# Optimization experiments

Measured on AMD Instinct MI355X. Metric: run time of the kernel, lower is better.

## Reference

```python
import jax, jax.numpy as jnp
import numpy as np

BATCH = 131072
FEAS = 256
K = 256
DEPTH = 3


def setup_inputs() -> dict:
    key = jax.random.key(0)
    ks = jax.random.split(key, 16)
    # deep tower dims: k//1 -> k//2 -> k//3 -> k//4  == 256 -> 128 -> 85 -> 64
    dims = [K // i for i in range(1, DEPTH + 2)]
    inp = {
        "x": jax.random.normal(ks[0], (BATCH, FEAS), jnp.float32),
        "w_wide": jax.random.normal(ks[1], (FEAS, 1), jnp.float32) * 0.02,
        "b_wide": jnp.zeros((1,), jnp.float32),
        # nn.Parameter(torch.rand(feas, k)) -> uniform [0,1)
        "V": jax.random.uniform(ks[2], (FEAS, K), jnp.float32),
    }
    for i in range(DEPTH):
        fan_in, fan_out = dims[i], dims[i + 1]
        inp[f"w{i+1}"] = jax.random.normal(ks[3 + 2 * i], (fan_in, fan_out), jnp.float32) * (1.0 / np.sqrt(fan_in))
        inp[f"b{i+1}"] = jnp.zeros((fan_out,), jnp.float32)
    inp["w_out"] = jax.random.normal(ks[12], (dims[-1], 1), jnp.float32) * (1.0 / np.sqrt(dims[-1]))
    inp["b_out"] = jnp.zeros((1,), jnp.float32)
    return inp


def reference(x, w_wide, b_wide, V, w1, b1, w2, b2, w3, b3, w_out, b_out):
    # wide (linear) part: [B, 1]
    linear = x @ w_wide + b_wide
    # FM bi-interaction pooling. Original loop: sum_{j >= i} x_i x_j (v_i * v_j)
    # (break/continue on zeros only skip zero-valued terms). Including the
    # diagonal, this equals 0.5 * ((x @ V)^2 + (x^2) @ (V^2)).  [B, K]
    xv = x @ V
    x2v2 = (x * x) @ (V * V)
    tmp = 0.5 * (xv * xv + x2v2)
    # deep tower: Linear + ReLU at each depth
    for w, b in ((w1, b1), (w2, b2), (w3, b3)):
        tmp = jax.nn.relu(tmp @ w + b)
    deep_out = tmp @ w_out + b_out  # [B, 1]
    return jax.nn.sigmoid(linear + deep_out)
```

## Files before the change

kernel.cpp:

```cpp
#include <hip/hip_runtime.h>
#include <math.h>


typedef _Float16 f16;
typedef _Float16 f16x4 __attribute__((ext_vector_type(4)));
typedef _Float16 f16x8 __attribute__((ext_vector_type(8)));
typedef float f32x4 __attribute__((ext_vector_type(4)));

#define NROWS   131072
#define ROWS    64
#define FDIM    256
#define KDIM    256
#define D1      128
#define D2      85
#define D2P     96

#define OFF_VT_H   0x0UL
#define OFF_VT_L   0x20000UL
#define OFF_V2T    0x40000UL
#define OFF_W1T_H  0x60000UL
#define OFF_W1T_L  0x70000UL
#define OFF_W2T_H  0x80000UL
#define OFF_W2T_L  0x86000UL
#define OFF_W3T_H  0x8C000UL
#define OFF_W3T_L  0x8F000UL

static __device__ __forceinline__ f32x4 mfma16(f16x8 a, f16x8 b, f32x4 c) {
  return __builtin_amdgcn_mfma_f32_16x16x32_f16(a, b, c, 0, 0, 0);
}

__global__ __launch_bounds__(256) void prep_kernel(
    const float* __restrict__ V, const float* __restrict__ w1,
    const float* __restrict__ w2, const float* __restrict__ w3,
    f16* VT_h, f16* VT_l, f16* V2T,
    f16* W1T_h, f16* W1T_l, f16* W2T_h, f16* W2T_l, f16* W3T_h, f16* W3T_l) {
  int idx0 = blockIdx.x * 256 + threadIdx.x;
  int stride = gridDim.x * 256;
  for (int idx = idx0; idx < KDIM * FDIM; idx += stride) {
    int k = idx >> 8, i = idx & 255;
    float v = V[i * KDIM + k];
    f16 h = (f16)v;
    VT_h[idx] = h;
    VT_l[idx] = (f16)(v - (float)h);
    V2T[idx] = (f16)(v * v);
  }
  for (int idx = idx0; idx < D1 * KDIM; idx += stride) {
    int n = idx >> 8, k = idx & 255;
    float w = w1[k * D1 + n];
    f16 h = (f16)w;
    W1T_h[idx] = h;
    W1T_l[idx] = (f16)(w - (float)h);
  }
  for (int idx = idx0; idx < D2P * D1; idx += stride) {
    int n = idx >> 7, k = idx & 127;
    float w = (n < D2) ? w2[k * D2 + n] : 0.f;
    f16 h = (f16)w;
    W2T_h[idx] = h;
    W2T_l[idx] = (f16)(w - (float)h);
  }
  for (int idx = idx0; idx < 64 * D2P; idx += stride) {
    int n = idx / D2P, k = idx - n * D2P;
    float w = (k < D2) ? w3[k * 64 + n] : 0.f;
    f16 h = (f16)w;
    W3T_h[idx] = h;
    W3T_l[idx] = (f16)(w - (float)h);
  }
}

__global__ __launch_bounds__(512, 4) void fused_kernel(
    const float* __restrict__ x, const float* __restrict__ w_wide,
    const float* __restrict__ b_wide,
    const f16* __restrict__ VT_h, const f16* __restrict__ VT_l,
    const f16* __restrict__ V2T,
    const f16* __restrict__ W1T_h, const f16* __restrict__ W1T_l,
    const float* __restrict__ b1,
    const f16* __restrict__ W2T_h, const f16* __restrict__ W2T_l,
    const float* __restrict__ b2,
    const f16* __restrict__ W3T_h, const f16* __restrict__ W3T_l,
    const float* __restrict__ b3,
    const float* __restrict__ w_out, const float* __restrict__ b_out,
    float* __restrict__ out) {
  __shared__ __align__(16) f16 smem[32768];
  __shared__ float linS[ROWS];
  __shared__ float pfS[ROWS * 2];

  f16* tmpH = smem;
  f16* tmpL = smem + 16384;
  f16* sXh  = smem;
  f16* sXl  = smem + 2560;
  f16* sX2  = smem + 5120;
  f16* h1H  = smem + 16384;
  f16* h1L  = smem + 24576;
  f16* h2H  = smem;
  f16* h2L  = smem + 8192;

  const int tid = threadIdx.x;
  const int lane = tid & 63, wv = tid >> 6;
  const int q = lane >> 4, ln = lane & 15;
  const int row0 = blockIdx.x * ROWS;
  const int sr = tid >> 3, sc = (tid & 7) * 4;

  f32x4 accV[4][2], acc2[4][2];
#pragma unroll
  for (int i = 0; i < 4; ++i)
#pragma unroll
    for (int j = 0; j < 2; ++j) {
      accV[i][j] = (f32x4){0.f, 0.f, 0.f, 0.f};
      acc2[i][j] = (f32x4){0.f, 0.f, 0.f, 0.f};
    }
  float linp = 0.f;

  const float* xrow = x + (size_t)(row0 + sr) * FDIM + sc;
  float4 a_cur = *(const float4*)(xrow);
  float4 w_cur = *(const float4*)(w_wide + sc);

  for (int ks = 0; ks < 8; ++ks) {
    const int k0 = ks * 32;
    __syncthreads();
    {
      float f0[4] = {a_cur.x, a_cur.y, a_cur.z, a_cur.w};
      f16x4 h0, l0, q0;
#pragma unroll
      for (int j = 0; j < 4; ++j) {
        f16 h = (f16)f0[j];
        h0[j] = h;
        l0[j] = (f16)(f0[j] - (float)h);
        q0[j] = (f16)(f0[j] * f0[j]);
      }
      int off0 = sr * 40 + sc;
      *(f16x4*)(sXh + off0) = h0;
      *(f16x4*)(sXl + off0) = l0;
      *(f16x4*)(sX2 + off0) = q0;
    }
    __syncthreads();

    float4 a_nxt = a_cur, w_nxt = w_cur;
    if (ks < 7) {
      a_nxt = *(const float4*)(xrow + k0 + 32);
      w_nxt = *(const float4*)(w_wide + k0 + 32 + sc);
    }
    linp += a_cur.x * w_cur.x + a_cur.y * w_cur.y + a_cur.z * w_cur.z +
            a_cur.w * w_cur.w;

    f16x8 Bh[2], Bl[2], B2[2];
#pragma unroll
    for (int ni = 0; ni < 2; ++ni) {
      int n = wv * 32 + ni * 16 + ln;
      size_t boff = (size_t)n * FDIM + k0 + q * 8;
      Bh[ni] = *(const f16x8*)(VT_h + boff);
      Bl[ni] = *(const f16x8*)(VT_l + boff);
      B2[ni] = *(const f16x8*)(V2T + boff);
    }
#pragma unroll
    for (int mi = 0; mi < 4; ++mi) {
      int off = (mi * 16 + ln) * 40 + q * 8;
      f16x8 Ah = *(const f16x8*)(sXh + off);
      f16x8 Al = *(const f16x8*)(sXl + off);
      f16x8 A2 = *(const f16x8*)(sX2 + off);
#pragma unroll
      for (int ni = 0; ni < 2; ++ni) {
        accV[mi][ni] = mfma16(Al, Bh[ni], accV[mi][ni]);
        accV[mi][ni] = mfma16(Ah, Bl[ni], accV[mi][ni]);
        accV[mi][ni] = mfma16(Ah, Bh[ni], accV[mi][ni]);
        acc2[mi][ni] = mfma16(A2, B2[ni], acc2[mi][ni]);
      }
    }
    a_cur = a_nxt;
    w_cur = w_nxt;
  }

  {
    float s0 = linp;
    s0 += __shfl_xor(s0, 1);
    s0 += __shfl_xor(s0, 2);
    s0 += __shfl_xor(s0, 4);
    if ((tid & 7) == 0) linS[sr] = s0 + b_wide[0];
  }

  __syncthreads();

#pragma unroll
  for (int mi = 0; mi < 4; ++mi)
#pragma unroll
    for (int r = 0; r < 4; ++r) {
      int m = mi * 16 + q * 4 + r;
      int mrow = m * 256, msw = m & 7;
#pragma unroll
      for (int ni = 0; ni < 2; ++ni) {
        int n = wv * 32 + ni * 16 + ln;
        float xv = accV[mi][ni][r];
        float val = 0.5f * (xv * xv + acc2[mi][ni][r]);
        f16 hi = (f16)val;
        f16 lo = (f16)(val - (float)hi);
        int off = mrow + (((n >> 3) ^ msw) << 3) + (n & 7);
        tmpH[off] = hi;
        tmpL[off] = lo;
      }
    }

  __syncthreads();

  f32x4 acc1[4];
#pragma unroll
  for (int i = 0; i < 4; ++i) acc1[i] = (f32x4){0.f, 0.f, 0.f, 0.f};

#pragma unroll
  for (int ks = 0; ks < 8; ++ks) {
    size_t boff = (size_t)(wv * 16 + ln) * KDIM + ks * 32 + q * 8;
    f16x8 Bh = *(const f16x8*)(W1T_h + boff);
    f16x8 Bl = *(const f16x8*)(W1T_l + boff);
#pragma unroll
    for (int mi = 0; mi < 4; ++mi) {
      int m = mi * 16 + ln;
      int aoff = m * 256 + (((ks * 4 + q) ^ (m & 7)) << 3);
      f16x8 Ah = *(const f16x8*)(tmpH + aoff);
      f16x8 Al = *(const f16x8*)(tmpL + aoff);
      acc1[mi] = mfma16(Al, Bh, acc1[mi]);
      acc1[mi] = mfma16(Ah, Bl, acc1[mi]);
      acc1[mi] = mfma16(Ah, Bh, acc1[mi]);
    }
  }

  __syncthreads();

  {
    int n = wv * 16 + ln;
    float bias = b1[n];
#pragma unroll
    for (int mi = 0; mi < 4; ++mi)
#pragma unroll
      for (int r = 0; r < 4; ++r) {
        int m = mi * 16 + q * 4 + r;
        float z = acc1[mi][r] + bias;
        z = z > 0.f ? z : 0.f;
        f16 hi = (f16)z;
        f16 lo = (f16)(z - (float)hi);
        int off = m * 128 + (((n >> 3) ^ (m & 7)) << 3) + (n & 7);
        h1H[off] = hi;
        h1L[off] = lo;
      }
  }

  __syncthreads();

  const int mt = wv & 3, half = wv >> 2;
  f32x4 accL2[3];
#pragma unroll
  for (int j = 0; j < 3; ++j) accL2[j] = (f32x4){0.f, 0.f, 0.f, 0.f};

#pragma unroll
  for (int ks = 0; ks < 4; ++ks) {
    int m = mt * 16 + ln;
    int aoff = m * 128 + (((ks * 4 + q) ^ (m & 7)) << 3);
    f16x8 Ah = *(const f16x8*)(h1H + aoff);
    f16x8 Al = *(const f16x8*)(h1L + aoff);
#pragma unroll
    for (int nj = 0; nj < 3; ++nj) {
      int n = (half * 3 + nj) * 16 + ln;
      size_t boff = (size_t)n * D1 + ks * 32 + q * 8;
      f16x8 Bh = *(const f16x8*)(W2T_h + boff);
      f16x8 Bl = *(const f16x8*)(W2T_l + boff);
      accL2[nj] = mfma16(Al, Bh, accL2[nj]);
      accL2[nj] = mfma16(Ah, Bl, accL2[nj]);
      accL2[nj] = mfma16(Ah, Bh, accL2[nj]);
    }
  }

#pragma unroll
  for (int r = 0; r < 4; ++r) {
    int m = mt * 16 + q * 4 + r;
    int mrow = m * 128, msw = m & 7;
#pragma unroll
    for (int nj = 0; nj < 3; ++nj) {
      int n = (half * 3 + nj) * 16 + ln;
      float z = accL2[nj][r] + ((n < D2) ? b2[n] : 0.f);
      z = z > 0.f ? z : 0.f;
      f16 hi = (f16)z;
      f16 lo = (f16)(z - (float)hi);
      int off = mrow + (((n >> 3) ^ msw) << 3) + (n & 7);
      h2H[off] = hi;
      h2L[off] = lo;
    }
  }

  __syncthreads();

  f32x4 accL3[2];
  accL3[0] = (f32x4){0.f, 0.f, 0.f, 0.f};
  accL3[1] = (f32x4){0.f, 0.f, 0.f, 0.f};

#pragma unroll
  for (int ks = 0; ks < 3; ++ks) {
    int m = mt * 16 + ln;
    int aoff = m * 128 + (((ks * 4 + q) ^ (m & 7)) << 3);
    f16x8 Ah = *(const f16x8*)(h2H + aoff);
    f16x8 Al = *(const f16x8*)(h2L + aoff);
#pragma unroll
    for (int nj = 0; nj < 2; ++nj) {
      int n = (half * 2 + nj) * 16 + ln;
      size_t boff = (size_t)n * D2P + ks * 32 + q * 8;
      f16x8 Bh = *(const f16x8*)(W3T_h + boff);
      f16x8 Bl = *(const f16x8*)(W3T_l + boff);
      accL3[nj] = mfma16(Al, Bh, accL3[nj]);
      accL3[nj] = mfma16(Ah, Bl, accL3[nj]);
      accL3[nj] = mfma16(Ah, Bh, accL3[nj]);
    }
  }

  {
    float b3v[2], wov[2];
#pragma unroll
    for (int nj = 0; nj < 2; ++nj) {
      int n = (half * 2 + nj) * 16 + ln;
      b3v[nj] = b3[n];
      wov[nj] = w_out[n];
    }
#pragma unroll
    for (int r = 0; r < 4; ++r) {
      float part = 0.f;
#pragma unroll
      for (int nj = 0; nj < 2; ++nj) {
        float z = accL3[nj][r] + b3v[nj];
        part += (z > 0.f ? z : 0.f) * wov[nj];
      }
      part += __shfl_xor(part, 1);
      part += __shfl_xor(part, 2);
      part += __shfl_xor(part, 4);
      part += __shfl_xor(part, 8);
      if (ln == 0) pfS[(mt * 16 + q * 4 + r) * 2 + half] = part;
    }
  }

  __syncthreads();

  if (tid < ROWS) {
    float zf = linS[tid] + pfS[tid * 2] + pfS[tid * 2 + 1] + b_out[0];
    out[row0 + tid] = 1.f / (1.f + expf(-zf));
  }
}

extern "C" void kernel_launch(void* const* d_in, const int* in_sizes, int n_in,
                              void* d_out, int out_size, void* d_ws, size_t ws_size,
                              hipStream_t stream) {
  const float* x = (const float*)d_in[0];
  const float* w_wide = (const float*)d_in[1];
  const float* b_wide = (const float*)d_in[2];
  const float* V = (const float*)d_in[3];
  const float* w1 = (const float*)d_in[4];
  const float* b1 = (const float*)d_in[5];
  const float* w2 = (const float*)d_in[6];
  const float* b2 = (const float*)d_in[7];
  const float* w3 = (const float*)d_in[8];
  const float* b3 = (const float*)d_in[9];
  const float* w_out = (const float*)d_in[10];
  const float* b_out = (const float*)d_in[11];
  float* out = (float*)d_out;
  char* ws = (char*)d_ws;

  f16* VT_h = (f16*)(ws + OFF_VT_H);
  f16* VT_l = (f16*)(ws + OFF_VT_L);
  f16* V2T = (f16*)(ws + OFF_V2T);
  f16* W1T_h = (f16*)(ws + OFF_W1T_H);
  f16* W1T_l = (f16*)(ws + OFF_W1T_L);
  f16* W2T_h = (f16*)(ws + OFF_W2T_H);
  f16* W2T_l = (f16*)(ws + OFF_W2T_L);
  f16* W3T_h = (f16*)(ws + OFF_W3T_H);
  f16* W3T_l = (f16*)(ws + OFF_W3T_L);

  prep_kernel<<<64, 256, 0, stream>>>(V, w1, w2, w3, VT_h, VT_l, V2T, W1T_h,
                                      W1T_l, W2T_h, W2T_l, W3T_h, W3T_l);

  fused_kernel<<<NROWS / ROWS, 512, 0, stream>>>(
      x, w_wide, b_wide, VT_h, VT_l, V2T, W1T_h, W1T_l, b1, W2T_h, W2T_l, b2,
      W3T_h, W3T_l, b3, w_out, b_out, out);
}
```

Before: 405.0 us.

## Restructure fused FM kernel: 32-row tiles, direct-to-LDS x load, packed hi/lo smem

The fused kernel now handles 32 rows per block with 256 threads instead of 64 rows with 512. Each block stages its whole x tile into LDS using global_load_lds and then converts it to fp16 hi/lo in registers, which removes the per-k-step conversion and double barrier. Intermediate activations are stored as packed hi/lo u32 pairs in padded rows rather than XOR-swizzled separate arrays. The work split per wave also changes (64 output columns per wave in the FM stage, with W2 padded to 128), at the cost of fewer rows sharing each B-fragment load and more weight traffic per row.

```diff
diff --git a/kernel.cpp b/kernel.cpp
--- a/kernel.cpp
+++ b/kernel.cpp
@@ -3,17 +3,17 @@
 
 
 typedef _Float16 f16;
-typedef _Float16 f16x4 __attribute__((ext_vector_type(4)));
 typedef _Float16 f16x8 __attribute__((ext_vector_type(8)));
 typedef float f32x4 __attribute__((ext_vector_type(4)));
+typedef unsigned int u32;
+typedef u32 u32x4 __attribute__((ext_vector_type(4)));
 
 #define NROWS   131072
-#define ROWS    64
+#define ROWS    32
 #define FDIM    256
 #define KDIM    256
 #define D1      128
 #define D2      85
-#define D2P     96
 
 #define OFF_VT_H   0x0UL
 #define OFF_VT_L   0x20000UL
@@ -21,12 +21,33 @@
 #define OFF_W1T_H  0x60000UL
 #define OFF_W1T_L  0x70000UL
 #define OFF_W2T_H  0x80000UL
-#define OFF_W2T_L  0x86000UL
-#define OFF_W3T_H  0x8C000UL
-#define OFF_W3T_L  0x8F000UL
+#define OFF_W2T_L  0x88000UL
+#define OFF_W3T_H  0x90000UL
+#define OFF_W3T_L  0x93000UL
 
 static __device__ __forceinline__ f32x4 mfma16(f16x8 a, f16x8 b, f32x4 c) {
   return __builtin_amdgcn_mfma_f32_16x16x32_f16(a, b, c, 0, 0, 0);
+}
+
+static __device__ __forceinline__ u32 pack2(float v) {
+  f16 hi = (f16)v;
+  f16 lo = (f16)(v - (float)hi);
+  union { f16 f[2]; u32 u; } t;
+  t.f[0] = hi;
+  t.f[1] = lo;
+  return t.u;
+}
+
+static __device__ __forceinline__ void unpack8(u32x4 a, u32x4 b, f16x8* H,
+                                               f16x8* L) {
+  union { u32 u; f16 f[2]; } t;
+  u32 w[8] = {a.x, a.y, a.z, a.w, b.x, b.y, b.z, b.w};
+#pragma unroll
+  for (int j = 0; j < 8; ++j) {
+    t.u = w[j];
+    (*H)[j] = t.f[0];
+    (*L)[j] = t.f[1];
+  }
 }
 
 __global__ __launch_bounds__(256) void prep_kernel(
@@ -51,15 +72,15 @@
     W1T_h[idx] = h;
     W1T_l[idx] = (f16)(w - (float)h);
   }
-  for (int idx = idx0; idx < D2P * D1; idx += stride) {
+  for (int idx = idx0; idx < 128 * 128; idx += stride) {
     int n = idx >> 7, k = idx & 127;
     float w = (n < D2) ? w2[k * D2 + n] : 0.f;
     f16 h = (f16)w;
     W2T_h[idx] = h;
     W2T_l[idx] = (f16)(w - (float)h);
   }
-  for (int idx = idx0; idx < 64 * D2P; idx += stride) {
-    int n = idx / D2P, k = idx - n * D2P;
+  for (int idx = idx0; idx < 64 * 96; idx += stride) {
+    int n = idx / 96, k = idx - n * 96;
     float w = (k < D2) ? w3[k * 64 + n] : 0.f;
     f16 h = (f16)w;
     W3T_h[idx] = h;
@@ -67,7 +88,7 @@
   }
 }
 
-__global__ __launch_bounds__(512, 4) void fused_kernel(
+__global__ __launch_bounds__(256, 3) void fused_kernel(
     const float* __restrict__ x, const float* __restrict__ w_wide,
     const float* __restrict__ b_wide,
     const f16* __restrict__ VT_h, const f16* __restrict__ VT_l,
@@ -80,261 +101,262 @@
     const float* __restrict__ b3,
     const float* __restrict__ w_out, const float* __restrict__ b_out,
     float* __restrict__ out) {
-  __shared__ __align__(16) f16 smem[32768];
+  __shared__ __align__(16) u32 arena[32 * 260 + 32 * 132];
   __shared__ float linS[ROWS];
-  __shared__ float pfS[ROWS * 2];
-
-  f16* tmpH = smem;
-  f16* tmpL = smem + 16384;
-  f16* sXh  = smem;
-  f16* sXl  = smem + 2560;
-  f16* sX2  = smem + 5120;
-  f16* h1H  = smem + 16384;
-  f16* h1L  = smem + 24576;
-  f16* h2H  = smem;
-  f16* h2L  = smem + 8192;
+  __shared__ float pfS[ROWS * 4];
 
   const int tid = threadIdx.x;
   const int lane = tid & 63, wv = tid >> 6;
   const int q = lane >> 4, ln = lane & 15;
   const int row0 = blockIdx.x * ROWS;
-  const int sr = tid >> 3, sc = (tid & 7) * 4;
-
-  f32x4 accV[4][2], acc2[4][2];
-#pragma unroll
-  for (int i = 0; i < 4; ++i)
-#pragma unroll
-    for (int j = 0; j < 2; ++j) {
+
+  {
+    const int r = wv * 8;
+#pragma unroll
+    for (int i = 0; i < 8; ++i) {
+      const float* src = x + (size_t)(row0 + r + i) * FDIM + (lane << 2);
+      float* dst = (float*)arena + (size_t)(r + i) * 260;
+      __builtin_amdgcn_global_load_lds(
+          (const __attribute__((address_space(1))) u32*)src,
+          (__attribute__((address_space(3))) u32*)dst, 16, 0, 0);
+    }
+  }
+  __syncthreads();
+
+  {
+    int lr = tid >> 3, lj = tid & 7;
+    const float* xrow = (const float*)arena + lr * 260 + lj * 4;
+    float lp = 0.f;
+#pragma unroll
+    for (int t = 0; t < 8; ++t) {
+      float4 v = *(const float4*)(xrow + t * 32);
+      float4 w = *(const float4*)(w_wide + lj * 4 + t * 32);
+      lp += v.x * w.x + v.y * w.y + v.z * w.z + v.w * w.w;
+    }
+    lp += __shfl_xor(lp, 1);
+    lp += __shfl_xor(lp, 2);
+    lp += __shfl_xor(lp, 4);
+    if (lj == 0) linS[lr] = lp + b_wide[0];
+  }
+
+  f32x4 accV[2][4], acc2[2][4];
+#pragma unroll
+  for (int i = 0; i < 2; ++i)
+#pragma unroll
+    for (int j = 0; j < 4; ++j) {
       accV[i][j] = (f32x4){0.f, 0.f, 0.f, 0.f};
       acc2[i][j] = (f32x4){0.f, 0.f, 0.f, 0.f};
     }
-  float linp = 0.f;
-
-  const float* xrow = x + (size_t)(row0 + sr) * FDIM + sc;
-  float4 a_cur = *(const float4*)(xrow);
-  float4 w_cur = *(const float4*)(w_wide + sc);
-
-  for (int ks = 0; ks < 8; ++ks) {
-    const int k0 = ks * 32;
-    __syncthreads();
-    {
-      float f0[4] = {a_cur.x, a_cur.y, a_cur.z, a_cur.w};
-      f16x4 h0, l0, q0;
-#pragma unroll
-      for (int j = 0; j < 4; ++j) {
-        f16 h = (f16)f0[j];
-        h0[j] = h;
-        l0[j] = (f16)(f0[j] - (float)h);
-        q0[j] = (f16)(f0[j] * f0[j]);
-      }
-      int off0 = sr * 40 + sc;
-      *(f16x4*)(sXh + off0) = h0;
-      *(f16x4*)(sXl + off0) = l0;
-      *(f16x4*)(sX2 + off0) = q0;
-    }
-    __syncthreads();
-
-    float4 a_nxt = a_cur, w_nxt = w_cur;
-    if (ks < 7) {
-      a_nxt = *(const float4*)(xrow + k0 + 32);
-      w_nxt = *(const float4*)(w_wide + k0 + 32 + sc);
-    }
-    linp += a_cur.x * w_cur.x + a_cur.y * w_cur.y + a_cur.z * w_cur.z +
-            a_cur.w * w_cur.w;
-
-    f16x8 Bh[2], Bl[2], B2[2];
-#pragma unroll
-    for (int ni = 0; ni < 2; ++ni) {
-      int n = wv * 32 + ni * 16 + ln;
-      size_t boff = (size_t)n * FDIM + k0 + q * 8;
-      Bh[ni] = *(const f16x8*)(VT_h + boff);
-      Bl[ni] = *(const f16x8*)(VT_l + boff);
-      B2[ni] = *(const f16x8*)(V2T + boff);
-    }
-#pragma unroll
-    for (int mi = 0; mi < 4; ++mi) {
-      int off = (mi * 16 + ln) * 40 + q * 8;
-      f16x8 Ah = *(const f16x8*)(sXh + off);
-      f16x8 Al = *(const f16x8*)(sXl + off);
-      f16x8 A2 = *(const f16x8*)(sX2 + off);
-#pragma unroll
-      for (int ni = 0; ni < 2; ++ni) {
-        accV[mi][ni] = mfma16(Al, Bh[ni], accV[mi][ni]);
-        accV[mi][ni] = mfma16(Ah, Bl[ni], accV[mi][ni]);
-        accV[mi][ni] = mfma16(Ah, Bh[ni], accV[mi][ni]);
-        acc2[mi][ni] = mfma16(A2, B2[ni], acc2[mi][ni]);
-      }
-    }
-    a_cur = a_nxt;
-    w_cur = w_nxt;
-  }
-
-  {
-    float s0 = linp;
-    s0 += __shfl_xor(s0, 1);
-    s0 += __shfl_xor(s0, 2);
-    s0 += __shfl_xor(s0, 4);
-    if ((tid & 7) == 0) linS[sr] = s0 + b_wide[0];
-  }
-
-  __syncthreads();
-
-#pragma unroll
-  for (int mi = 0; mi < 4; ++mi)
-#pragma unroll
-    for (int r = 0; r < 4; ++r) {
-      int m = mi * 16 + q * 4 + r;
-      int mrow = m * 256, msw = m & 7;
-#pragma unroll
-      for (int ni = 0; ni < 2; ++ni) {
-        int n = wv * 32 + ni * 16 + ln;
-        float xv = accV[mi][ni][r];
-        float val = 0.5f * (xv * xv + acc2[mi][ni][r]);
-        f16 hi = (f16)val;
-        f16 lo = (f16)(val - (float)hi);
-        int off = mrow + (((n >> 3) ^ msw) << 3) + (n & 7);
-        tmpH[off] = hi;
-        tmpL[off] = lo;
-      }
-    }
-
-  __syncthreads();
-
-  f32x4 acc1[4];
-#pragma unroll
-  for (int i = 0; i < 4; ++i) acc1[i] = (f32x4){0.f, 0.f, 0.f, 0.f};
-
-#pragma unroll
-  for (int ks = 0; ks < 8; ++ks) {
-    size_t boff = (size_t)(wv * 16 + ln) * KDIM + ks * 32 + q * 8;
-    f16x8 Bh = *(const f16x8*)(W1T_h + boff);
-    f16x8 Bl = *(const f16x8*)(W1T_l + boff);
-#pragma unroll
-    for (int mi = 0; mi < 4; ++mi) {
-      int m = mi * 16 + ln;
-      int aoff = m * 256 + (((ks * 4 + q) ^ (m & 7)) << 3);
-      f16x8 Ah = *(const f16x8*)(tmpH + aoff);
-      f16x8 Al = *(const f16x8*)(tmpL + aoff);
-      acc1[mi] = mfma16(Al, Bh, acc1[mi]);
-      acc1[mi] = mfma16(Ah, Bl, acc1[mi]);
-      acc1[mi] = mfma16(Ah, Bh, acc1[mi]);
-    }
-  }
-
-  __syncthreads();
-
-  {
-    int n = wv * 16 + ln;
-    float bias = b1[n];
-#pragma unroll
-    for (int mi = 0; mi < 4; ++mi)
+  {
+    const float* xS = (const float*)arena;
+#pragma unroll 1
+    for (int ks = 0; ks < 8; ++ks) {
+      const int k0 = ks * 32;
+      f16x8 Bh[4], Bl[4], B2[4];
+#pragma unroll
+      for (int ni = 0; ni < 4; ++ni) {
+        int n = wv * 64 + ni * 16 + ln;
+        size_t boff = (size_t)n * FDIM + k0 + q * 8;
+        Bh[ni] = *(const f16x8*)(VT_h + boff);
+        Bl[ni] = *(const f16x8*)(VT_l + boff);
+        B2[ni] = *(const f16x8*)(V2T + boff);
+      }
+#pragma unroll
+      for (int mi = 0; mi < 2; ++mi) {
+        const float* xp = xS + (mi * 16 + ln) * 260 + k0 + q * 8;
+        float4 r0 = *(const float4*)(xp);
+        float4 r1 = *(const float4*)(xp + 4);
+        float f[8] = {r0.x, r0.y, r0.z, r0.w, r1.x, r1.y, r1.z, r1.w};
+        f16x8 Ah, Al, A2;
+#pragma unroll
+        for (int j = 0; j < 8; ++j) {
+          f16 h = (f16)f[j];
+          Ah[j] = h;
+          Al[j] = (f16)(f[j] - (float)h);
+          A2[j] = (f16)(f[j] * f[j]);
+        }
+#pragma unroll
+        for (int ni = 0; ni < 4; ++ni) {
+          accV[mi][ni] = mfma16(Al, Bh[ni], accV[mi][ni]);
+          accV[mi][ni] = mfma16(Ah, Bl[ni], accV[mi][ni]);
+          accV[mi][ni] = mfma16(Ah, Bh[ni], accV[mi][ni]);
+          acc2[mi][ni] = mfma16(A2, B2[ni], acc2[mi][ni]);
+        }
+      }
+    }
+  }
+  __syncthreads();
+
+  {
+    u32* tmpS = arena;
+#pragma unroll
+    for (int mi = 0; mi < 2; ++mi)
 #pragma unroll
       for (int r = 0; r < 4; ++r) {
         int m = mi * 16 + q * 4 + r;
-        float z = acc1[mi][r] + bias;
-        z = z > 0.f ? z : 0.f;
-        f16 hi = (f16)z;
-        f16 lo = (f16)(z - (float)hi);
-        int off = m * 128 + (((n >> 3) ^ (m & 7)) << 3) + (n & 7);
-        h1H[off] = hi;
-        h1L[off] = lo;
-      }
-  }
-
-  __syncthreads();
-
-  const int mt = wv & 3, half = wv >> 2;
-  f32x4 accL2[3];
-#pragma unroll
-  for (int j = 0; j < 3; ++j) accL2[j] = (f32x4){0.f, 0.f, 0.f, 0.f};
-
-#pragma unroll
-  for (int ks = 0; ks < 4; ++ks) {
-    int m = mt * 16 + ln;
-    int aoff = m * 128 + (((ks * 4 + q) ^ (m & 7)) << 3);
-    f16x8 Ah = *(const f16x8*)(h1H + aoff);
-    f16x8 Al = *(const f16x8*)(h1L + aoff);
-#pragma unroll
-    for (int nj = 0; nj < 3; ++nj) {
-      int n = (half * 3 + nj) * 16 + ln;
-      size_t boff = (size_t)n * D1 + ks * 32 + q * 8;
-      f16x8 Bh = *(const f16x8*)(W2T_h + boff);
-      f16x8 Bl = *(const f16x8*)(W2T_l + boff);
-      accL2[nj] = mfma16(Al, Bh, accL2[nj]);
-      accL2[nj] = mfma16(Ah, Bl, accL2[nj]);
-      accL2[nj] = mfma16(Ah, Bh, accL2[nj]);
-    }
-  }
-
-#pragma unroll
-  for (int r = 0; r < 4; ++r) {
-    int m = mt * 16 + q * 4 + r;
-    int mrow = m * 128, msw = m & 7;
-#pragma unroll
-    for (int nj = 0; nj < 3; ++nj) {
-      int n = (half * 3 + nj) * 16 + ln;
-      float z = accL2[nj][r] + ((n < D2) ? b2[n] : 0.f);
-      z = z > 0.f ? z : 0.f;
-      f16 hi = (f16)z;
-      f16 lo = (f16)(z - (float)hi);
-      int off = mrow + (((n >> 3) ^ msw) << 3) + (n & 7);
-      h2H[off] = hi;
-      h2L[off] = lo;
-    }
-  }
-
-  __syncthreads();
-
-  f32x4 accL3[2];
-  accL3[0] = (f32x4){0.f, 0.f, 0.f, 0.f};
-  accL3[1] = (f32x4){0.f, 0.f, 0.f, 0.f};
-
-#pragma unroll
-  for (int ks = 0; ks < 3; ++ks) {
-    int m = mt * 16 + ln;
-    int aoff = m * 128 + (((ks * 4 + q) ^ (m & 7)) << 3);
-    f16x8 Ah = *(const f16x8*)(h2H + aoff);
-    f16x8 Al = *(const f16x8*)(h2L + aoff);
-#pragma unroll
-    for (int nj = 0; nj < 2; ++nj) {
-      int n = (half * 2 + nj) * 16 + ln;
-      size_t boff = (size_t)n * D2P + ks * 32 + q * 8;
+        u32* rowp = tmpS + m * 260;
+#pragma unroll
+        for (int ni = 0; ni < 4; ++ni) {
+          int n = wv * 64 + ni * 16 + ln;
+          float xv = accV[mi][ni][r];
+          rowp[n] = pack2(0.5f * (xv * xv + acc2[mi][ni][r]));
+        }
+      }
+  }
+  __syncthreads();
+
+  f32x4 acc1[2][2];
+#pragma unroll
+  for (int i = 0; i < 2; ++i) {
+    acc1[i][0] = (f32x4){0.f, 0.f, 0.f, 0.f};
+    acc1[i][1] = (f32x4){0.f, 0.f, 0.f, 0.f};
+  }
+  {
+    const u32* tmpS = arena;
+#pragma unroll 1
+    for (int ks = 0; ks < 8; ++ks) {
+      const int k0 = ks * 32;
+      f16x8 Bh[2], Bl[2];
+#pragma unroll
+      for (int nj = 0; nj < 2; ++nj) {
+        int n = wv * 32 + nj * 16 + ln;
+        size_t boff = (size_t)n * KDIM + k0 + q * 8;
+        Bh[nj] = *(const f16x8*)(W1T_h + boff);
+        Bl[nj] = *(const f16x8*)(W1T_l + boff);
+      }
+#pragma unroll
+      for (int mi = 0; mi < 2; ++mi) {
+        const u32* tp = tmpS + (mi * 16 + ln) * 260 + k0 + q * 8;
+        u32x4 p0 = *(const u32x4*)(tp);
+        u32x4 p1 = *(const u32x4*)(tp + 4);
+        f16x8 Ah, Al;
+        unpack8(p0, p1, &Ah, &Al);
+#pragma unroll
+        for (int nj = 0; nj < 2; ++nj) {
+          acc1[mi][nj] = mfma16(Al, Bh[nj], acc1[mi][nj]);
+          acc1[mi][nj] = mfma16(Ah, Bl[nj], acc1[mi][nj]);
+          acc1[mi][nj] = mfma16(Ah, Bh[nj], acc1[mi][nj]);
+        }
+      }
+    }
+  }
+  {
+    u32* h1S = arena + 32 * 260;
+#pragma unroll
+    for (int mi = 0; mi < 2; ++mi)
+#pragma unroll
+      for (int r = 0; r < 4; ++r) {
+        int m = mi * 16 + q * 4 + r;
+#pragma unroll
+        for (int nj = 0; nj < 2; ++nj) {
+          int n = wv * 32 + nj * 16 + ln;
+          float z = acc1[mi][nj][r] + b1[n];
+          h1S[m * 132 + n] = pack2(z > 0.f ? z : 0.f);
+        }
+      }
+  }
+  __syncthreads();
+
+  f32x4 accL2[2][2];
+#pragma unroll
+  for (int i = 0; i < 2; ++i) {
+    accL2[i][0] = (f32x4){0.f, 0.f, 0.f, 0.f};
+    accL2[i][1] = (f32x4){0.f, 0.f, 0.f, 0.f};
+  }
+  {
+    const u32* h1S = arena + 32 * 260;
+#pragma unroll 1
+    for (int ks = 0; ks < 4; ++ks) {
+      const int k0 = ks * 32;
+      f16x8 Bh[2], Bl[2];
+#pragma unroll
+      for (int nj = 0; nj < 2; ++nj) {
+        int n = wv * 32 + nj * 16 + ln;
+        size_t boff = (size_t)n * 128 + k0 + q * 8;
+        Bh[nj] = *(const f16x8*)(W2T_h + boff);
+        Bl[nj] = *(const f16x8*)(W2T_l + boff);
+      }
+#pragma unroll
+      for (int mi = 0; mi < 2; ++mi) {
+        const u32* hp = h1S + (mi * 16 + ln) * 132 + k0 + q * 8;
+        u32x4 p0 = *(const u32x4*)(hp);
+        u32x4 p1 = *(const u32x4*)(hp + 4);
+        f16x8 Ah, Al;
+        unpack8(p0, p1, &Ah, &Al);
+#pragma unroll
+        for (int nj = 0; nj < 2; ++nj) {
+          accL2[mi][nj] = mfma16(Al, Bh[nj], accL2[mi][nj]);
+          accL2[mi][nj] = mfma16(Ah, Bl[nj], accL2[mi][nj]);
+          accL2[mi][nj] = mfma16(Ah, Bh[nj], accL2[mi][nj]);
+        }
+      }
+    }
+  }
+  {
+    u32* h2S = arena;
+#pragma unroll
+    for (int mi = 0; mi < 2; ++mi)
+#pragma unroll
+      for (int r = 0; r < 4; ++r) {
+        int m = mi * 16 + q * 4 + r;
+#pragma unroll
+        for (int nj = 0; nj < 2; ++nj) {
+          int n = wv * 32 + nj * 16 + ln;
+          if (n < 96) {
+            float z = accL2[mi][nj][r] + ((n < D2) ? b2[n] : 0.f);
+            h2S[m * 100 + n] = pack2(z > 0.f ? z : 0.f);
+          }
+        }
+      }
+  }
+  __syncthreads();
+
+  f32x4 acc3[2];
+  acc3[0] = (f32x4){0.f, 0.f, 0.f, 0.f};
+  acc3[1] = (f32x4){0.f, 0.f, 0.f, 0.f};
+  {
+    const u32* h2S = arena;
+    const int n3 = wv * 16 + ln;
+#pragma unroll
+    for (int ks = 0; ks < 3; ++ks) {
+      const int k0 = ks * 32;
+      size_t boff = (size_t)n3 * 96 + k0 + q * 8;
       f16x8 Bh = *(const f16x8*)(W3T_h + boff);
       f16x8 Bl = *(const f16x8*)(W3T_l + boff);
-      accL3[nj] = mfma16(Al, Bh, accL3[nj]);
-      accL3[nj] = mfma16(Ah, Bl, accL3[nj]);
-      accL3[nj] = mfma16(Ah, Bh, accL3[nj]);
-    }
-  }
-
-  {
-    float b3v[2], wov[2];
-#pragma unroll
-    for (int nj = 0; nj < 2; ++nj) {
-      int n = (half * 2 + nj) * 16 + ln;
-      b3v[nj] = b3[n];
-      wov[nj] = w_out[n];
-    }
-#pragma unroll
-    for (int r = 0; r < 4; ++r) {
-      float part = 0.f;
-#pragma unroll
-      for (int nj = 0; nj < 2; ++nj) {
-        float z = accL3[nj][r] + b3v[nj];
-        part += (z > 0.f ? z : 0.f) * wov[nj];
-      }
-      part += __shfl_xor(part, 1);
-      part += __shfl_xor(part, 2);
-      part += __shfl_xor(part, 4);
-      part += __shfl_xor(part, 8);
-      if (ln == 0) pfS[(mt * 16 + q * 4 + r) * 2 + half] = part;
-    }
-  }
-
+#pragma unroll
+      for (int mi = 0; mi < 2; ++mi) {
+        const u32* hp = h2S + (mi * 16 + ln) * 100 + k0 + q * 8;
+        u32x4 p0 = *(const u32x4*)(hp);
+        u32x4 p1 = *(const u32x4*)(hp + 4);
+        f16x8 Ah, Al;
+        unpack8(p0, p1, &Ah, &Al);
+        acc3[mi] = mfma16(Al, Bh, acc3[mi]);
+        acc3[mi] = mfma16(Ah, Bl, acc3[mi]);
+        acc3[mi] = mfma16(Ah, Bh, acc3[mi]);
+      }
+    }
+  }
+  {
+    const int n3 = wv * 16 + ln;
+    float b3v = b3[n3], wov = w_out[n3];
+#pragma unroll
+    for (int mi = 0; mi < 2; ++mi)
+#pragma unroll
+      for (int r = 0; r < 4; ++r) {
+        float z = acc3[mi][r] + b3v;
+        float part = (z > 0.f ? z : 0.f) * wov;
+        part += __shfl_xor(part, 1);
+        part += __shfl_xor(part, 2);
+        part += __shfl_xor(part, 4);
+        part += __shfl_xor(part, 8);
+        if (ln == 0) pfS[(mi * 16 + q * 4 + r) * 4 + wv] = part;
+      }
+  }
   __syncthreads();
 
   if (tid < ROWS) {
-    float zf = linS[tid] + pfS[tid * 2] + pfS[tid * 2 + 1] + b_out[0];
+    float zf = linS[tid] + pfS[tid * 4] + pfS[tid * 4 + 1] + pfS[tid * 4 + 2] +
+               pfS[tid * 4 + 3] + b_out[0];
     out[row0 + tid] = 1.f / (1.f + expf(-zf));
   }
 }
@@ -370,7 +392,7 @@
   prep_kernel<<<64, 256, 0, stream>>>(V, w1, w2, w3, VT_h, VT_l, V2T, W1T_h,
                                       W1T_l, W2T_h, W2T_l, W3T_h, W3T_l);
 
-  fused_kernel<<<NROWS / ROWS, 512, 0, stream>>>(
+  fused_kernel<<<NROWS / ROWS, 256, 0, stream>>>(
       x, w_wide, b_wide, VT_h, VT_l, V2T, W1T_h, W1T_l, b1, W2T_h, W2T_l, b2,
       W3T_h, W3T_l, b3, w_out, b_out, out);
 }
```

Measured after the change: 476.4 us. 17.6% more time.
